# Optimization experiments

Measured on AMD Instinct MI355X. Metric: run time of the kernel, lower is better.

Reference implementation:

```python
import jax, jax.numpy as jnp
import numpy as np
from jax.scipy.special import logsumexp

B, N = 256, 65536
NEG_INF = jnp.float32(-1e30)  # acts as -inf for logsumexp, keeps grads finite


def setup_inputs() -> dict:
    key = jax.random.key(0)
    k1, k2 = jax.random.split(key)
    sim = jax.random.uniform(k1, (B, N), dtype=jnp.float32)
    label = jax.random.uniform(k2, (B, N), dtype=jnp.float32)
    return {"sim": sim, "label": label}


def _ranking_loss(sim, label):
    m = 0.2
    gamma = 64.0
    delta_p = 1.0 - m  # 0.8
    delta_n = m        # 0.2

    pos_mask = label > 0.5
    neg_mask = label < 0.25

    # ---- positives: logit_p = -relu(0.8 - sim).detach() * (sim - 0.8) * gamma ----
    alpha_p = jax.lax.stop_gradient(jnp.maximum(0.8 - sim, 0.0))
    logit_p = -alpha_p * (sim - delta_p) * gamma
    lse_p = logsumexp(jnp.where(pos_mask, logit_p, NEG_INF), axis=1)
    # torch fallback: no positives -> logit_p = [0.0], logsumexp == 0
    lse_p = jnp.where(pos_mask.any(axis=1), lse_p, 0.0)

    # ---- negatives: if >20 negatives, keep only top-10 largest sims ----
    alpha_n_all = jax.lax.stop_gradient(jnp.maximum(sim - 0.2, 0.0))
    logit_n_all = alpha_n_all * (sim - delta_n) * gamma
    lse_n_all = logsumexp(jnp.where(neg_mask, logit_n_all, NEG_INF), axis=1)

    neg_sim_masked = jnp.where(neg_mask, sim, NEG_INF)
    top_v, _ = jax.lax.top_k(neg_sim_masked, 10)  # [B, 10]
    alpha_n_top = jax.lax.stop_gradient(jnp.maximum(top_v - 0.2, 0.0))
    logit_n_top = alpha_n_top * (top_v - delta_n) * gamma
    lse_n_top = logsumexp(logit_n_top, axis=1)

    n_neg = neg_mask.sum(axis=1)
    lse_n = jnp.where(n_neg > 20, lse_n_top, lse_n_all)

    loss_loc = jax.nn.softplus(lse_n + lse_p).sum()
    return loss_loc / sim.shape[0]  # reduction='mean'


def reference(sim, label):
    return _ranking_loss(sim, label)
```

## Files before the change

### kernel.cpp

```cpp
#include <hip/hip_runtime.h>
#include <cmath>

#define NEG_INF (-1.0e30f)

static constexpr int B = 256;
static constexpr int N = 65536;
static constexpr int THREADS = 1024;
static constexpr float C_OFF = 40.96f;

__device__ __forceinline__ float wave_sum_f(float v) {
#pragma unroll
  for (int off = 32; off >= 1; off >>= 1) v += __shfl_xor(v, off, 64);
  return v;
}
__device__ __forceinline__ int wave_sum_i(int v) {
#pragma unroll
  for (int off = 32; off >= 1; off >>= 1) v += __shfl_xor(v, off, 64);
  return v;
}

__device__ __forceinline__ void merge_lists_shfl(float t[16], int off) {
  float b[16];
#pragma unroll
  for (int i = 0; i < 16; ++i) b[i] = __shfl_xor(t[i], off, 64);
  float c[16];
#pragma unroll
  for (int i = 0; i < 16; ++i) c[i] = fmaxf(t[i], b[15 - i]);
#pragma unroll
  for (int s = 8; s >= 1; s >>= 1) {
#pragma unroll
    for (int i = 0; i < 16; ++i) {
      if ((i & s) == 0) {
        float lo = c[i], hi = c[i + s];
        c[i] = fmaxf(lo, hi);
        c[i + s] = fminf(lo, hi);
      }
    }
  }
#pragma unroll
  for (int i = 0; i < 16; ++i) t[i] = c[i];
}

__device__ __forceinline__ void process_elem(float s, float l, float& s_p,
                                             float& s_n, int& nn, float t[16]) {
  const bool pos = l > 0.5f;
  const bool neg = l < 0.25f;
  float dp = 0.8f - s;
  float lp = (dp > 0.f) ? 64.f * dp * dp : 0.f;
  float dn = s - 0.2f;
  float ln_ = (dn > 0.f) ? 64.f * dn * dn : 0.f;
  float arg = pos ? (lp - C_OFF) : (neg ? (ln_ - C_OFF) : -1.0e30f);
  float e = __expf(arg);
  if (pos) s_p += e;
  if (neg) {
    s_n += e;
    ++nn;
    if (s > t[9]) {
      t[9] = s;
#pragma unroll
      for (int i = 9; i > 0; --i) {
        float a = t[i - 1], bb = t[i];
        t[i - 1] = fmaxf(a, bb);
        t[i] = fminf(a, bb);
      }
    }
  }
}

__global__ void __launch_bounds__(THREADS) ranking_row_kernel(
    const float* __restrict__ sim, const float* __restrict__ label,
    float* __restrict__ row_loss) {
  const int row = blockIdx.x;
  const int tid = threadIdx.x;
  const float4* sim4 = reinterpret_cast<const float4*>(sim) + (size_t)row * (N / 4);
  const float4* lab4 = reinterpret_cast<const float4*>(label) + (size_t)row * (N / 4);

  float s_p = 0.f, s_n = 0.f;
  int nn = 0;
  float t[16];
#pragma unroll
  for (int i = 0; i < 16; ++i) t[i] = NEG_INF;

  constexpr int ITER = N / 4 / THREADS;
#pragma unroll 4
  for (int it = 0; it < ITER; ++it) {
    float4 sv = sim4[it * THREADS + tid];
    float4 lv = lab4[it * THREADS + tid];
    process_elem(sv.x, lv.x, s_p, s_n, nn, t);
    process_elem(sv.y, lv.y, s_p, s_n, nn, t);
    process_elem(sv.z, lv.z, s_p, s_n, nn, t);
    process_elem(sv.w, lv.w, s_p, s_n, nn, t);
  }

  s_p = wave_sum_f(s_p);
  s_n = wave_sum_f(s_n);
  nn = wave_sum_i(nn);
#pragma unroll
  for (int off = 1; off < 64; off <<= 1) merge_lists_shfl(t, off);

  __shared__ float ls_p[16], ls_n[16];
  __shared__ int ls_c[16];
  __shared__ float ltop[16][16];
  const int wave = tid >> 6, lane = tid & 63;
  if (lane == 0) {
    ls_p[wave] = s_p;
    ls_n[wave] = s_n;
    ls_c[wave] = nn;
#pragma unroll
    for (int i = 0; i < 16; ++i) ltop[wave][i] = t[i];
  }
  __syncthreads();

  if (wave == 0) {
    float m[16];
    if (lane < 16) {
#pragma unroll
      for (int i = 0; i < 16; ++i) m[i] = ltop[lane][i];
    } else {
#pragma unroll
      for (int i = 0; i < 16; ++i) m[i] = NEG_INF;
    }
    merge_lists_shfl(m, 1);
    merge_lists_shfl(m, 2);
    merge_lists_shfl(m, 4);
    merge_lists_shfl(m, 8);

    float sp = (lane < 16) ? ls_p[lane] : 0.f;
    float sn = (lane < 16) ? ls_n[lane] : 0.f;
    int cn = (lane < 16) ? ls_c[lane] : 0;
    sp = wave_sum_f(sp);
    sn = wave_sum_f(sn);
    cn = wave_sum_i(cn);

    if (lane == 0) {
      float lse_p = (sp > 0.f) ? (C_OFF + __logf(sp)) : 0.f;
      float lse_n_all = (sn > 0.f) ? (C_OFF + __logf(sn)) : NEG_INF;

      float mx = NEG_INF;
      float lg[10];
#pragma unroll
      for (int i = 0; i < 10; ++i) {
        float v = m[i];
        float a = fmaxf(v - 0.2f, 0.f);
        float lo = a * (v - 0.2f) * 64.f;
        lg[i] = lo;
        mx = fmaxf(mx, lo);
      }
      float ss = 0.f;
#pragma unroll
      for (int i = 0; i < 10; ++i) ss += __expf(lg[i] - mx);
      float lse_n_top = mx + __logf(ss);

      float lse_n = (cn > 20) ? lse_n_top : lse_n_all;
      float x = lse_n + lse_p;
      float loss = fmaxf(x, 0.f) + log1pf(__expf(-fabsf(x)));
      row_loss[row] = loss;
    }
  }
}

__global__ void __launch_bounds__(256) final_reduce_kernel(
    const float* __restrict__ row_loss, float* __restrict__ out) {
  const int tid = threadIdx.x;
  float v = row_loss[tid];
  v = wave_sum_f(v);
  __shared__ float ws[4];
  if ((tid & 63) == 0) ws[tid >> 6] = v;
  __syncthreads();
  if (tid == 0) out[0] = (ws[0] + ws[1] + ws[2] + ws[3]) * (1.0f / 256.0f);
}

extern "C" void kernel_launch(void* const* d_in, const int* in_sizes, int n_in,
                              void* d_out, int out_size, void* d_ws, size_t ws_size,
                              hipStream_t stream) {
  const float* sim = (const float*)d_in[0];
  const float* label = (const float*)d_in[1];
  float* out = (float*)d_out;
  float* rows = (float*)d_ws;
  ranking_row_kernel<<<dim3(B), dim3(THREADS), 0, stream>>>(sim, label, rows);
  final_reduce_kernel<<<dim3(1), dim3(256), 0, stream>>>(rows, out);
}
```

Measured before the change: 155.8 us.

## Split rows into chunks and replace per-thread top-10 with thresholded candidate buffer

Each row is now split across four 512-thread blocks that write partial sums, counts and top-10 lists, and a final kernel merges them. The per-element register top-10 insertion is replaced by appending negatives with sim above 0.98 to a shared-memory buffer through atomics. If the buffer overflows or holds too few candidates, the block falls back to rescanning its chunk with exact per-thread top-10. The aim is to cut per-element ALU and register pressure and to raise grid parallelism. The cost is shared atomics contention and a possible second pass over the chunk.

```diff
diff --git a/kernel.cpp b/kernel.cpp
--- a/kernel.cpp
+++ b/kernel.cpp
@@ -5,8 +5,15 @@
 
 static constexpr int B = 256;
 static constexpr int N = 65536;
-static constexpr int THREADS = 1024;
+static constexpr int CHUNKS = 4;
+static constexpr int THREADS = 512;
+static constexpr int NBLOCKS = B * CHUNKS;
+static constexpr int CHUNK_ELEMS = N / CHUNKS;
+static constexpr int ITER = CHUNK_ELEMS / 4 / THREADS;
 static constexpr float C_OFF = 40.96f;
+static constexpr float CAND_THRESH = 0.98f;
+static constexpr int CAP = 1024;
+static constexpr int PSTRIDE = 16;
 
 __device__ __forceinline__ float wave_sum_f(float v) {
 #pragma unroll
@@ -17,6 +24,18 @@
 #pragma unroll
   for (int off = 32; off >= 1; off >>= 1) v += __shfl_xor(v, off, 64);
   return v;
+}
+
+__device__ __forceinline__ void insert10(float t[16], float s) {
+  if (s > t[9]) {
+    t[9] = s;
+#pragma unroll
+    for (int i = 9; i > 0; --i) {
+      float a = t[i - 1], b = t[i];
+      t[i - 1] = fmaxf(a, b);
+      t[i] = fminf(a, b);
+    }
+  }
 }
 
 __device__ __forceinline__ void merge_lists_shfl(float t[16], int off) {
@@ -41,133 +60,185 @@
   for (int i = 0; i < 16; ++i) t[i] = c[i];
 }
 
-__device__ __forceinline__ void process_elem(float s, float l, float& s_p,
-                                             float& s_n, int& nn, float t[16]) {
+__device__ __forceinline__ void proc(float s, float l, float& s_p, float& s_n,
+                                     int& nn, float* cand, int* cnt) {
   const bool pos = l > 0.5f;
   const bool neg = l < 0.25f;
-  float dp = 0.8f - s;
-  float lp = (dp > 0.f) ? 64.f * dp * dp : 0.f;
-  float dn = s - 0.2f;
-  float ln_ = (dn > 0.f) ? 64.f * dn * dn : 0.f;
-  float arg = pos ? (lp - C_OFF) : (neg ? (ln_ - C_OFF) : -1.0e30f);
-  float e = __expf(arg);
+  float d = pos ? (0.8f - s) : (s - 0.2f);
+  float r = fmaxf(d, 0.f);
+  float e = __expf(fmaf(64.f * r, r, -C_OFF));
   if (pos) s_p += e;
   if (neg) {
     s_n += e;
     ++nn;
-    if (s > t[9]) {
-      t[9] = s;
-#pragma unroll
-      for (int i = 9; i > 0; --i) {
-        float a = t[i - 1], bb = t[i];
-        t[i - 1] = fmaxf(a, bb);
-        t[i] = fminf(a, bb);
-      }
-    }
-  }
-}
-
-__global__ void __launch_bounds__(THREADS) ranking_row_kernel(
+    if (s > CAND_THRESH) {
+      int p = atomicAdd(cnt, 1);
+      if (p < CAP) cand[p] = s;
+    }
+  }
+}
+
+__global__ void __launch_bounds__(THREADS, 8) ranking_partial_kernel(
     const float* __restrict__ sim, const float* __restrict__ label,
-    float* __restrict__ row_loss) {
-  const int row = blockIdx.x;
+    float* __restrict__ partials) {
+  const int blk = blockIdx.x;
+  const int row = blk >> 2;
+  const int chunk = blk & 3;
   const int tid = threadIdx.x;
-  const float4* sim4 = reinterpret_cast<const float4*>(sim) + (size_t)row * (N / 4);
-  const float4* lab4 = reinterpret_cast<const float4*>(label) + (size_t)row * (N / 4);
+  const int wave = tid >> 6, lane = tid & 63;
+
+  __shared__ float cand[CAP];
+  __shared__ int cnt;
+  __shared__ float ls_p[8], ls_n[8];
+  __shared__ int ls_c[8];
+  __shared__ float ltop[8][16];
+  if (tid == 0) cnt = 0;
+  __syncthreads();
+
+  const size_t base4 =
+      (size_t)row * (N / 4) + (size_t)chunk * (CHUNK_ELEMS / 4);
+  const float4* sim4 = reinterpret_cast<const float4*>(sim) + base4;
+  const float4* lab4 = reinterpret_cast<const float4*>(label) + base4;
 
   float s_p = 0.f, s_n = 0.f;
   int nn = 0;
-  float t[16];
-#pragma unroll
-  for (int i = 0; i < 16; ++i) t[i] = NEG_INF;
-
-  constexpr int ITER = N / 4 / THREADS;
-#pragma unroll 4
+
+#pragma unroll 2
   for (int it = 0; it < ITER; ++it) {
     float4 sv = sim4[it * THREADS + tid];
     float4 lv = lab4[it * THREADS + tid];
-    process_elem(sv.x, lv.x, s_p, s_n, nn, t);
-    process_elem(sv.y, lv.y, s_p, s_n, nn, t);
-    process_elem(sv.z, lv.z, s_p, s_n, nn, t);
-    process_elem(sv.w, lv.w, s_p, s_n, nn, t);
+    proc(sv.x, lv.x, s_p, s_n, nn, cand, &cnt);
+    proc(sv.y, lv.y, s_p, s_n, nn, cand, &cnt);
+    proc(sv.z, lv.z, s_p, s_n, nn, cand, &cnt);
+    proc(sv.w, lv.w, s_p, s_n, nn, cand, &cnt);
   }
 
   s_p = wave_sum_f(s_p);
   s_n = wave_sum_f(s_n);
   nn = wave_sum_i(nn);
-#pragma unroll
-  for (int off = 1; off < 64; off <<= 1) merge_lists_shfl(t, off);
-
-  __shared__ float ls_p[16], ls_n[16];
-  __shared__ int ls_c[16];
-  __shared__ float ltop[16][16];
-  const int wave = tid >> 6, lane = tid & 63;
   if (lane == 0) {
     ls_p[wave] = s_p;
     ls_n[wave] = s_n;
     ls_c[wave] = nn;
-#pragma unroll
-    for (int i = 0; i < 16; ++i) ltop[wave][i] = t[i];
   }
   __syncthreads();
 
-  if (wave == 0) {
-    float m[16];
-    if (lane < 16) {
-#pragma unroll
-      for (int i = 0; i < 16; ++i) m[i] = ltop[lane][i];
-    } else {
-#pragma unroll
-      for (int i = 0; i < 16; ++i) m[i] = NEG_INF;
-    }
-    merge_lists_shfl(m, 1);
-    merge_lists_shfl(m, 2);
-    merge_lists_shfl(m, 4);
-    merge_lists_shfl(m, 8);
-
-    float sp = (lane < 16) ? ls_p[lane] : 0.f;
-    float sn = (lane < 16) ? ls_n[lane] : 0.f;
-    int cn = (lane < 16) ? ls_c[lane] : 0;
-    sp = wave_sum_f(sp);
-    sn = wave_sum_f(sn);
-    cn = wave_sum_i(cn);
-
+  float sp_tot = 0.f, sn_tot = 0.f;
+  int nn_tot = 0;
+#pragma unroll
+  for (int i = 0; i < 8; ++i) {
+    sp_tot += ls_p[i];
+    sn_tot += ls_n[i];
+    nn_tot += ls_c[i];
+  }
+  const int cnt_tot = cnt;
+  const bool bad = (cnt_tot > CAP) || (cnt_tot < 10 && cnt_tot < nn_tot);
+
+  float t[16];
+#pragma unroll
+  for (int i = 0; i < 16; ++i) t[i] = NEG_INF;
+
+  float* P = partials + (size_t)blk * PSTRIDE;
+
+  if (!bad) {
+    if (wave == 0) {
+      const int c = cnt_tot < CAP ? cnt_tot : CAP;
+      for (int i = lane; i < c; i += 64) insert10(t, cand[i]);
+#pragma unroll
+      for (int off = 1; off < 64; off <<= 1) merge_lists_shfl(t, off);
+      if (lane == 0) {
+        P[0] = sp_tot;
+        P[1] = sn_tot;
+        P[2] = (float)nn_tot;
+        P[3] = 0.f;
+#pragma unroll
+        for (int i = 0; i < 10; ++i) P[4 + i] = t[i];
+      }
+    }
+  } else {
+    for (int it = 0; it < ITER; ++it) {
+      float4 sv = sim4[it * THREADS + tid];
+      float4 lv = lab4[it * THREADS + tid];
+      if (lv.x < 0.25f) insert10(t, sv.x);
+      if (lv.y < 0.25f) insert10(t, sv.y);
+      if (lv.z < 0.25f) insert10(t, sv.z);
+      if (lv.w < 0.25f) insert10(t, sv.w);
+    }
+#pragma unroll
+    for (int off = 1; off < 64; off <<= 1) merge_lists_shfl(t, off);
     if (lane == 0) {
-      float lse_p = (sp > 0.f) ? (C_OFF + __logf(sp)) : 0.f;
-      float lse_n_all = (sn > 0.f) ? (C_OFF + __logf(sn)) : NEG_INF;
-
-      float mx = NEG_INF;
-      float lg[10];
-#pragma unroll
-      for (int i = 0; i < 10; ++i) {
-        float v = m[i];
-        float a = fmaxf(v - 0.2f, 0.f);
-        float lo = a * (v - 0.2f) * 64.f;
-        lg[i] = lo;
-        mx = fmaxf(mx, lo);
-      }
-      float ss = 0.f;
-#pragma unroll
-      for (int i = 0; i < 10; ++i) ss += __expf(lg[i] - mx);
-      float lse_n_top = mx + __logf(ss);
-
-      float lse_n = (cn > 20) ? lse_n_top : lse_n_all;
-      float x = lse_n + lse_p;
-      float loss = fmaxf(x, 0.f) + log1pf(__expf(-fabsf(x)));
-      row_loss[row] = loss;
-    }
-  }
-}
-
-__global__ void __launch_bounds__(256) final_reduce_kernel(
-    const float* __restrict__ row_loss, float* __restrict__ out) {
-  const int tid = threadIdx.x;
-  float v = row_loss[tid];
-  v = wave_sum_f(v);
+#pragma unroll
+      for (int i = 0; i < 16; ++i) ltop[wave][i] = t[i];
+    }
+    __syncthreads();
+    if (wave == 0) {
+      float m[16];
+      if (lane < 8) {
+#pragma unroll
+        for (int i = 0; i < 16; ++i) m[i] = ltop[lane][i];
+      } else {
+#pragma unroll
+        for (int i = 0; i < 16; ++i) m[i] = NEG_INF;
+      }
+      merge_lists_shfl(m, 1);
+      merge_lists_shfl(m, 2);
+      merge_lists_shfl(m, 4);
+      if (lane == 0) {
+        P[0] = sp_tot;
+        P[1] = sn_tot;
+        P[2] = (float)nn_tot;
+        P[3] = 0.f;
+#pragma unroll
+        for (int i = 0; i < 10; ++i) P[4 + i] = m[i];
+      }
+    }
+  }
+}
+
+__global__ void __launch_bounds__(256) final_kernel(
+    const float* __restrict__ partials, float* __restrict__ out) {
+  const int r = threadIdx.x;
+  float sp = 0.f, sn = 0.f, nnf = 0.f;
+  float t[16];
+#pragma unroll
+  for (int i = 0; i < 16; ++i) t[i] = NEG_INF;
+#pragma unroll
+  for (int c = 0; c < CHUNKS; ++c) {
+    const float* P = partials + (size_t)(r * CHUNKS + c) * PSTRIDE;
+    sp += P[0];
+    sn += P[1];
+    nnf += P[2];
+#pragma unroll
+    for (int i = 0; i < 10; ++i) insert10(t, P[4 + i]);
+  }
+
+  float lse_p = (sp > 0.f) ? (C_OFF + __logf(sp)) : 0.f;
+  float lse_n_all = (sn > 0.f) ? (C_OFF + __logf(sn)) : NEG_INF;
+
+  float mx = NEG_INF;
+  float lg[10];
+#pragma unroll
+  for (int i = 0; i < 10; ++i) {
+    float v = t[i];
+    float a = fmaxf(v - 0.2f, 0.f);
+    float lo = a * (v - 0.2f) * 64.f;
+    lg[i] = lo;
+    mx = fmaxf(mx, lo);
+  }
+  float ss = 0.f;
+#pragma unroll
+  for (int i = 0; i < 10; ++i) ss += __expf(lg[i] - mx);
+  float lse_n_top = mx + __logf(ss);
+
+  float lse_n = (nnf > 20.5f) ? lse_n_top : lse_n_all;
+  float x = lse_n + lse_p;
+  float loss = fmaxf(x, 0.f) + log1pf(__expf(-fabsf(x)));
+
+  loss = wave_sum_f(loss);
   __shared__ float ws[4];
-  if ((tid & 63) == 0) ws[tid >> 6] = v;
+  if ((r & 63) == 0) ws[r >> 6] = loss;
   __syncthreads();
-  if (tid == 0) out[0] = (ws[0] + ws[1] + ws[2] + ws[3]) * (1.0f / 256.0f);
+  if (r == 0) out[0] = (ws[0] + ws[1] + ws[2] + ws[3]) * (1.0f / 256.0f);
 }
 
 extern "C" void kernel_launch(void* const* d_in, const int* in_sizes, int n_in,
@@ -176,7 +247,7 @@
   const float* sim = (const float*)d_in[0];
   const float* label = (const float*)d_in[1];
   float* out = (float*)d_out;
-  float* rows = (float*)d_ws;
-  ranking_row_kernel<<<dim3(B), dim3(THREADS), 0, stream>>>(sim, label, rows);
-  final_reduce_kernel<<<dim3(1), dim3(256), 0, stream>>>(rows, out);
-}
+  float* partials = (float*)d_ws;
+  ranking_partial_kernel<<<dim3(NBLOCKS), dim3(THREADS), 0, stream>>>(sim, label, partials);
+  final_kernel<<<dim3(1), dim3(256), 0, stream>>>(partials, out);
+}
```

Result: no change. 156.1 us (+0.2%).
